# Kernel tuning notes

Measured on AMD Instinct MI355X. Metric: run time of the kernel, lower is better.

## Reference

```python
import jax, jax.numpy as jnp
import numpy as np

GAMMA = 0.3      # LinearSpike surrogate slope (Bellec et al. 2018)
TIMESTEPS = 8
DROPOUT = 0.2

@jax.custom_vjp
def spike_fn(mem_thr):
    # forward: Heaviside spike; backward: piecewise-linear surrogate
    return (mem_thr > 0).astype(mem_thr.dtype)

def _spike_fwd(m):
    return (m > 0).astype(m.dtype), m

def _spike_bwd(m, g):
    return (GAMMA * jnp.maximum(1.0 - jnp.abs(m), 0.0) * g,)

spike_fn.defvjp(_spike_fwd, _spike_bwd)

def conv(x, w, stride=1, pad=1):
    return jax.lax.conv_general_dilated(
        x, w, (stride, stride), [(pad, pad), (pad, pad)],
        dimension_numbers=('NCHW', 'OIHW', 'NCHW'))

def avgpool2(x):
    B, C, H, W = x.shape
    return x.reshape(B, C, H // 2, 2, W // 2, 2).mean(axis=(3, 5))

def lif(mem, delta, leak, thr):
    mem = leak * mem + delta                  # leaky integrate
    mem_thr = mem / thr - 1.0                 # normalized membrane
    out = spike_fn(mem_thr)                   # binary spike
    mem = mem - thr * (mem_thr > 0).astype(mem.dtype)  # soft reset
    return mem, out

def setup_inputs() -> dict:
    key = jax.random.key(0)
    ks = jax.random.split(key, 24)
    B = 32
    def w(k, o, i, kh):
        std = float(np.sqrt(2.0 / (kh * kh * o)))  # matches _initialize_weights2
        return jax.random.normal(k, (o, i, kh, kh), jnp.float32) * std
    def mask(k, shape):
        keep = jax.random.bernoulli(k, 1.0 - DROPOUT, shape)
        return keep.astype(jnp.float32) / (1.0 - DROPOUT)
    return {
        'x': jax.random.normal(ks[0], (B, 3, 32, 32), jnp.float32),
        'w_pre0': w(ks[1], 64, 3, 3),
        'w_pre1': w(ks[2], 64, 64, 3),
        'w_pre2': w(ks[3], 64, 64, 3),
        'w1a': w(ks[4], 64, 64, 3),  'w1b': w(ks[5], 64, 64, 3),
        'w2a': w(ks[6], 128, 64, 3), 'w2b': w(ks[7], 128, 128, 3), 'w2i': w(ks[8], 128, 64, 1),
        'w3a': w(ks[9], 256, 128, 3), 'w3b': w(ks[10], 256, 256, 3), 'w3i': w(ks[11], 256, 128, 1),
        'w4a': w(ks[12], 512, 256, 3), 'w4b': w(ks[13], 512, 512, 3), 'w4i': w(ks[14], 512, 256, 1),
        'w_fc': jax.random.normal(ks[15], (10, 512 * 2 * 2), jnp.float32) * 0.01,
        'thr': jnp.ones((11,), jnp.float32),
        'leak': jnp.ones((11,), jnp.float32),
        'mask2': mask(ks[16], (B, 64, 32, 32)),
        'mask5': mask(ks[17], (B, 64, 32, 32)),
        'mask9': mask(ks[18], (B, 64, 16, 16)),
        'mask11': mask(ks[19], (B, 128, 8, 8)),
        'mask13': mask(ks[20], (B, 256, 4, 4)),
        'mask15': mask(ks[21], (B, 512, 2, 2)),
    }

def _forward(x, w_pre0, w_pre1, w_pre2, w1a, w1b, w2a, w2b, w2i,
             w3a, w3b, w3i, w4a, w4b, w4i, w_fc, thr, leak,
             mask2, mask5, mask9, mask11, mask13, mask15):
    B = x.shape[0]
    f32 = jnp.float32
    mems0 = (
        jnp.zeros((B, 64, 32, 32), f32), jnp.zeros((B, 64, 32, 32), f32),
        jnp.zeros((B, 64, 32, 32), f32),
        jnp.zeros((B, 64, 16, 16), f32), jnp.zeros((B, 64, 16, 16), f32),
        jnp.zeros((B, 128, 8, 8), f32), jnp.zeros((B, 128, 8, 8), f32),
        jnp.zeros((B, 256, 4, 4), f32), jnp.zeros((B, 256, 4, 4), f32),
        jnp.zeros((B, 512, 2, 2), f32), jnp.zeros((B, 512, 2, 2), f32),
        jnp.zeros((B, 10), f32),  # output accumulator mem
    )

    def step(carry, _):
        m0, m1, m2, m3, m4, m5, m6, m7, m8, m9, m10, mfc = carry
        # pre_process: (conv->spike->dropout) x2, conv->spike, avgpool2
        m0, o = lif(m0, conv(x, w_pre0), leak[0], thr[0]); o = o * mask2
        m1, o = lif(m1, conv(o, w_pre1), leak[1], thr[1]); o = o * mask5
        m2, o = lif(m2, conv(o, w_pre2), leak[2], thr[2])
        o = avgpool2(o)  # 32x32 -> 16x16
        # layer1 BasicBlock (stride 1, identity shortcut)
        inp = o
        m3, o = lif(m3, conv(inp, w1a), leak[3], thr[3]); o = o * mask9
        m4, o = lif(m4, conv(o, w1b) + inp, leak[4], thr[4])
        # layer2 BasicBlock (stride 2, 1x1 conv shortcut)
        inp = o
        m5, o = lif(m5, conv(inp, w2a, stride=2), leak[5], thr[5]); o = o * mask11
        m6, o = lif(m6, conv(o, w2b) + conv(inp, w2i, stride=2, pad=0), leak[6], thr[6])
        # layer3
        inp = o
        m7, o = lif(m7, conv(inp, w3a, stride=2), leak[7], thr[7]); o = o * mask13
        m8, o = lif(m8, conv(o, w3b) + conv(inp, w3i, stride=2, pad=0), leak[8], thr[8])
        # layer4
        inp = o
        m9, o = lif(m9, conv(inp, w4a, stride=2), leak[9], thr[9]); o = o * mask15
        m10, o = lif(m10, conv(o, w4b) + conv(inp, w4i, stride=2, pad=0), leak[10], thr[10])
        # output layer: pure accumulation of classifier current over timesteps
        mfc = mfc + o.reshape(B, -1) @ w_fc.T
        return (m0, m1, m2, m3, m4, m5, m6, m7, m8, m9, m10, mfc), None

    carry, _ = jax.lax.scan(step, mems0, None, length=TIMESTEPS)
    return carry[-1]  # [B, labels]

def reference(x, w_pre0, w_pre1, w_pre2, w1a, w1b, w2a, w2b, w2i,
              w3a, w3b, w3i, w4a, w4b, w4i, w_fc, thr, leak,
              mask2, mask5, mask9, mask11, mask13, mask15):
    return _forward(x, w_pre0, w_pre1, w_pre2, w1a, w1b, w2a, w2b, w2i,
                    w3a, w3b, w3i, w4a, w4b, w4i, w_fc, thr, leak,
                    mask2, mask5, mask9, mask11, mask13, mask15)
```

## Files before the change

kernel.cpp:

```cpp
#include <hip/hip_runtime.h>

#define BATCH 32

template<int H, int KS>
__global__ __launch_bounds__(256) void conv64_v2(
    const float* __restrict__ in, const float* __restrict__ w,
    float* __restrict__ pbuf)
{
    constexpr int W    = H;
    constexpr int QR   = W / 4;
    constexpr int ROWS = 64 / QR;
    constexpr int RS   = W + 4;
    constexpr int CC   = 8;
    constexpr int PLANE = (ROWS + 2) * RS;
    constexpr int CCT  = 64 / KS;
    constexpr int NCH  = CCT / CC;
    constexpr int NTOT = 32 * 64 * H * W;
    __shared__ float sIn[CC * PLANE];

    const int tid  = threadIdx.x;
    const int b    = blockIdx.x;
    const int rt   = blockIdx.y;
    const int zc   = blockIdx.z;
    const int cg   = zc & 1;
    const int ks   = zc >> 1;
    const int lane = tid & 63;
    const int g    = __builtin_amdgcn_readfirstlane(tid >> 6);
    const int octet = cg * 32 + g * 8;
    const int r    = lane / QR;
    const int wq   = lane % QR;
    const int ho   = rt * ROWS + r;
    const int row0 = rt * ROWS;

    float acc[8][4] = {};
    const size_t in_b = (size_t)b * 64 * H * W;

    for (int ch = 0; ch < NCH; ++ch) {
        const int c0 = ks * CCT + ch * CC;
        if (ch) __syncthreads();
        constexpr int LCNT = CC * (ROWS + 2) * (W + 2);
        for (int i = tid; i < LCNT; i += 256) {
            int c   = i / ((ROWS + 2) * (W + 2));
            int rr  = (i / (W + 2)) % (ROWS + 2);
            int col = i % (W + 2);
            int ih  = row0 + rr - 1;
            int iw  = col - 1;
            float v = 0.f;
            if ((unsigned)ih < (unsigned)H && (unsigned)iw < (unsigned)W)
                v = in[in_b + (size_t)(c0 + c) * H * W + ih * W + iw];
            sIn[c * PLANE + rr * RS + col] = v;
        }
        __syncthreads();

        for (int c = 0; c < CC; ++c) {
            float rv[3][6];
            #pragma unroll
            for (int dr = 0; dr < 3; ++dr) {
                const float* p = &sIn[c * PLANE + (r + dr) * RS + wq * 4];
                float4 a  = *(const float4*)p;
                float2 b2 = *(const float2*)(p + 4);
                rv[dr][0] = a.x;  rv[dr][1] = a.y; rv[dr][2] = a.z; rv[dr][3] = a.w;
                rv[dr][4] = b2.x; rv[dr][5] = b2.y;
            }
            const float* wc = w + ((size_t)octet * 64 + (c0 + c)) * 9;
            #pragma unroll
            for (int j = 0; j < 8; ++j) {
                const float* wk = wc + (size_t)j * 64 * 9;
                float w0 = wk[0], w1 = wk[1], w2 = wk[2];
                float w3 = wk[3], w4 = wk[4], w5 = wk[5];
                float w6 = wk[6], w7 = wk[7], w8 = wk[8];
                #pragma unroll
                for (int k = 0; k < 4; ++k) {
                    acc[j][k] = fmaf(rv[0][k + 0], w0, acc[j][k]);
                    acc[j][k] = fmaf(rv[0][k + 1], w1, acc[j][k]);
                    acc[j][k] = fmaf(rv[0][k + 2], w2, acc[j][k]);
                    acc[j][k] = fmaf(rv[1][k + 0], w3, acc[j][k]);
                    acc[j][k] = fmaf(rv[1][k + 1], w4, acc[j][k]);
                    acc[j][k] = fmaf(rv[1][k + 2], w5, acc[j][k]);
                    acc[j][k] = fmaf(rv[2][k + 0], w6, acc[j][k]);
                    acc[j][k] = fmaf(rv[2][k + 1], w7, acc[j][k]);
                    acc[j][k] = fmaf(rv[2][k + 2], w8, acc[j][k]);
                }
            }
        }
    }

    #pragma unroll
    for (int j = 0; j < 8; ++j) {
        const size_t idx = ((size_t)(b * 64 + octet + j) * H + ho) * W + wq * 4;
        *(float4*)&pbuf[(size_t)ks * NTOT + idx] =
            make_float4(acc[j][0], acc[j][1], acc[j][2], acc[j][3]);
    }
}

template<int CI, int CO, int KS, int RT>
__global__ __launch_bounds__(256) void conv_mid(
    const float* __restrict__ in,
    const float* __restrict__ w,
    float* __restrict__ pbuf)
{
    constexpr int HIN = 16, HOUT = 8;
    constexpr int CC  = CI / KS;
    constexpr int NR  = (RT - 1) * 2 + 3;
    constexpr int BSTR = NR * HIN + 4;
    constexpr int CST  = 32 * BSTR;
    constexpr int NTOT = 32 * CO * HOUT * HOUT;
    __shared__ float sBuf[CC * CST];

    const int tid  = threadIdx.x;
    const int lane = tid & 63;
    const int b    = lane >> 1;
    const int ks   = blockIdx.x;
    const int co_u = __builtin_amdgcn_readfirstlane(blockIdx.y * 4 + (tid >> 6));
    const int r0   = blockIdx.z * RT;
    const int g0   = r0 * 2 - 1;

    for (int i = tid; i < CC * 32 * NR * 4; i += 256) {
        int q  = i % 4;
        int s  = (i / 4) % NR;
        int bb = (i / (4 * NR)) % 32;
        int c  = i / (4 * NR * 32);
        int gr = g0 + s;
        float4 v = make_float4(0.f, 0.f, 0.f, 0.f);
        if ((unsigned)gr < (unsigned)HIN)
            v = *(const float4*)&in[(((size_t)bb * CI + ks * CC + c) * HIN + gr) * HIN + q * 4];
        *(float4*)&sBuf[c * CST + bb * BSTR + s * HIN + q * 4] = v;
    }
    __syncthreads();

    float acc[RT * 8] = {};
    #pragma unroll 2
    for (int c = 0; c < CC; ++c) {
        const float* wk = w + ((size_t)co_u * CI + ks * CC + c) * 9;
        float wr[9];
        #pragma unroll
        for (int q = 0; q < 9; ++q) wr[q] = wk[q];
        float pl[NR * HIN];
        #pragma unroll
        for (int k = 0; k < NR * 4; ++k) {
            float4 v = *(const float4*)&sBuf[c * CST + b * BSTR + k * 4];
            pl[k * 4 + 0] = v.x; pl[k * 4 + 1] = v.y;
            pl[k * 4 + 2] = v.z; pl[k * 4 + 3] = v.w;
        }
        #pragma unroll
        for (int j = 0; j < RT; ++j) {
            #pragma unroll
            for (int ow = 0; ow < 8; ++ow) {
                #pragma unroll
                for (int kh = 0; kh < 3; ++kh) {
                    const int s = 2 * j + kh;
                    #pragma unroll
                    for (int kw = 0; kw < 3; ++kw) {
                        const int iw = 2 * ow - 1 + kw;
                        if (iw < 0 || iw >= HIN) continue;
                        acc[j * 8 + ow] = fmaf(pl[s * HIN + iw], wr[kh * 3 + kw],
                                               acc[j * 8 + ow]);
                    }
                }
            }
        }
    }

    if ((lane & 1) == 0) {
        #pragma unroll
        for (int j = 0; j < RT; ++j) {
            const size_t idx = ((size_t)(b * CO + co_u) * HOUT + r0 + j) * HOUT;
            *(float4*)&pbuf[(size_t)ks * NTOT + idx]     =
                make_float4(acc[j * 8 + 0], acc[j * 8 + 1], acc[j * 8 + 2], acc[j * 8 + 3]);
            *(float4*)&pbuf[(size_t)ks * NTOT + idx + 4] =
                make_float4(acc[j * 8 + 4], acc[j * 8 + 5], acc[j * 8 + 6], acc[j * 8 + 7]);
        }
    }
}

template<int KS>
__global__ __launch_bounds__(256) void conv_l2b(
    const float* __restrict__ in,
    const float* __restrict__ w,
    const float* __restrict__ sc_in,
    const float* __restrict__ sc_w,
    float* __restrict__ pbuf)
{
    constexpr int CI = 128, CO = 128, SC_CI = 64;
    constexpr int CC  = CI / KS;
    constexpr int SCC = SC_CI / KS;
    constexpr int BSTR = 52;
    constexpr int CST  = 32 * BSTR;
    constexpr int BSTRs = 36;
    constexpr int CSTs  = 32 * BSTRs;
    constexpr int NTOT = 32 * CO * 64;
    __shared__ float sBuf[CC * CST];

    const int tid  = threadIdx.x;
    const int lane = tid & 63;
    const int b    = lane >> 1;
    const int co_u = __builtin_amdgcn_readfirstlane(blockIdx.y * 4 + (tid >> 6));
    const int ks   = blockIdx.x;
    const int sp   = blockIdx.z;
    const int r0   = sp * 4;

    for (int i = tid; i < CC * 32 * 12; i += 256) {
        int f4  = i % 2;
        int row = (i / 2) % 6;
        int bb  = (i / 12) % 32;
        int c   = i / 384;
        int gr  = r0 - 1 + row;
        float4 v = make_float4(0.f, 0.f, 0.f, 0.f);
        if ((unsigned)gr < 8u)
            v = *(const float4*)&in[(((size_t)bb * CI + ks * CC + c) * 8 + gr) * 8 + f4 * 4];
        *(float4*)&sBuf[c * CST + bb * BSTR + row * 8 + f4 * 4] = v;
    }
    __syncthreads();

    float acc[32] = {};
    #pragma unroll 2
    for (int c = 0; c < CC; ++c) {
        const float* wk = w + ((size_t)co_u * CI + ks * CC + c) * 9;
        float wr[9];
        #pragma unroll
        for (int q = 0; q < 9; ++q) wr[q] = wk[q];
        float pl[48];
        #pragma unroll
        for (int k = 0; k < 12; ++k) {
            float4 v = *(const float4*)&sBuf[c * CST + b * BSTR + k * 4];
            pl[k * 4 + 0] = v.x; pl[k * 4 + 1] = v.y;
            pl[k * 4 + 2] = v.z; pl[k * 4 + 3] = v.w;
        }
        #pragma unroll
        for (int oh = 0; oh < 4; ++oh) {
            #pragma unroll
            for (int ow = 0; ow < 8; ++ow) {
                #pragma unroll
                for (int kh = 0; kh < 3; ++kh) {
                    #pragma unroll
                    for (int kw = 0; kw < 3; ++kw) {
                        const int iw = ow - 1 + kw;
                        if (iw < 0 || iw >= 8) continue;
                        acc[oh * 8 + ow] = fmaf(pl[(oh + kh) * 8 + iw],
                                                wr[kh * 3 + kw], acc[oh * 8 + ow]);
                    }
                }
            }
        }
    }
    __syncthreads();

    for (int i = tid; i < SCC * 32 * 16; i += 256) {
        int q   = i % 4;
        int row = (i / 4) % 4;
        int bb  = (i / 16) % 32;
        int c   = i / 512;
        float4 v = *(const float4*)&sc_in[
            (((size_t)bb * SC_CI + ks * SCC + c) * 16 + 2 * (r0 + row)) * 16 + q * 4];
        sBuf[c * CSTs + bb * BSTRs + row * 8 + q * 2 + 0] = v.x;
        sBuf[c * CSTs + bb * BSTRs + row * 8 + q * 2 + 1] = v.z;
    }
    __syncthreads();

    #pragma unroll
    for (int c = 0; c < SCC; ++c) {
        float sw = sc_w[(size_t)co_u * SC_CI + ks * SCC + c];
        #pragma unroll
        for (int p4 = 0; p4 < 8; ++p4) {
            float4 v = *(const float4*)&sBuf[c * CSTs + b * BSTRs + p4 * 4];
            acc[p4 * 4 + 0] = fmaf(v.x, sw, acc[p4 * 4 + 0]);
            acc[p4 * 4 + 1] = fmaf(v.y, sw, acc[p4 * 4 + 1]);
            acc[p4 * 4 + 2] = fmaf(v.z, sw, acc[p4 * 4 + 2]);
            acc[p4 * 4 + 3] = fmaf(v.w, sw, acc[p4 * 4 + 3]);
        }
    }

    if ((lane & 1) == 0) {
        #pragma unroll
        for (int oh = 0; oh < 4; ++oh) {
            const size_t idx = ((size_t)(b * CO + co_u) * 8 + r0 + oh) * 8;
            *(float4*)&pbuf[(size_t)ks * NTOT + idx]     =
                make_float4(acc[oh * 8 + 0], acc[oh * 8 + 1], acc[oh * 8 + 2], acc[oh * 8 + 3]);
            *(float4*)&pbuf[(size_t)ks * NTOT + idx + 4] =
                make_float4(acc[oh * 8 + 4], acc[oh * 8 + 5], acc[oh * 8 + 6], acc[oh * 8 + 7]);
        }
    }
}

template<int CI, int HIN, int STRIDE, int CO, int SC_CI, int SC_HIN,
         int KS, int COB>
__global__ __launch_bounds__(COB * 64) void conv_ks(
    const float* __restrict__ in, const float* __restrict__ w,
    const float* __restrict__ sc_in, const float* __restrict__ sc_w,
    float* __restrict__ pbuf)
{
    constexpr int NT   = COB * 64;
    constexpr int HOUT = (STRIDE == 2) ? HIN / 2 : HIN;
    constexpr int P    = HOUT * HOUT;
    constexpr int NPIX = HIN * HIN;
    constexpr int CC   = CI / KS;
    constexpr int SCC  = (SC_CI > 0) ? SC_CI / KS : 0;
    constexpr int BSTR = NPIX + (((NPIX / 4) % 2 == 0) ? 4 : 0);
    constexpr int CST  = 32 * BSTR;
    constexpr int BSTRs = P + (((P / 4) % 2 == 0) ? 4 : 0);
    constexpr int CSTs  = 32 * BSTRs;
    static_assert(CI % KS == 0, "ks split");
    static_assert(NPIX % 4 == 0 && P % 4 == 0, "vector widths");

    __shared__ float sIn[CC * CST];
    __shared__ float sSc[(SCC > 0) ? SCC * CSTs : 1];

    const int tid  = threadIdx.x;
    const int lane = tid & 63;
    const int b    = lane >> 1;
    const int ks   = blockIdx.x;
    const int co_u = __builtin_amdgcn_readfirstlane(blockIdx.y * COB + (tid >> 6));
    const int cb   = ks * CC;

    constexpr int NF4 = CC * 32 * (NPIX / 4);
    for (int i = tid; i < NF4; i += NT) {
        int k4 = i % (NPIX / 4);
        int c  = (i / (NPIX / 4)) % CC;
        int bb = i / ((NPIX / 4) * CC);
        float4 v = *(const float4*)&in[((size_t)bb * CI + cb + c) * NPIX + k4 * 4];
        *(float4*)&sIn[c * CST + bb * BSTR + k4 * 4] = v;
    }
    if constexpr (SCC > 0) {
        constexpr int NH  = HOUT / 2;
        constexpr int NSC = SCC * 32 * HOUT * NH;
        for (int i = tid; i < NSC; i += NT) {
            int hc = i % NH;
            int r  = (i / NH) % HOUT;
            int c  = (i / (NH * HOUT)) % SCC;
            int bb = i / (NH * HOUT * SCC);
            float4 v = *(const float4*)&sc_in[
                ((size_t)(bb * SC_CI + ks * SCC + c) * SC_HIN + 2 * r) * SC_HIN
                + hc * 4];
            sSc[c * CSTs + bb * BSTRs + r * HOUT + hc * 2 + 0] = v.x;
            sSc[c * CSTs + bb * BSTRs + r * HOUT + hc * 2 + 1] = v.z;
        }
    }
    __syncthreads();

    float acc[P] = {};

    const float* wbase = w + ((size_t)co_u * CI + cb) * 9;
    #pragma unroll 4
    for (int j = 0; j < CC; ++j) {
        float wr[9];
        #pragma unroll
        for (int q = 0; q < 9; ++q) wr[q] = wbase[j * 9 + q];
        float plane[NPIX];
        #pragma unroll
        for (int r4 = 0; r4 < NPIX / 4; ++r4) {
            float4 v = *(const float4*)&sIn[j * CST + b * BSTR + r4 * 4];
            plane[r4 * 4 + 0] = v.x; plane[r4 * 4 + 1] = v.y;
            plane[r4 * 4 + 2] = v.z; plane[r4 * 4 + 3] = v.w;
        }
        #pragma unroll
        for (int ho = 0; ho < HOUT; ++ho) {
            #pragma unroll
            for (int wo = 0; wo < HOUT; ++wo) {
                #pragma unroll
                for (int kh = 0; kh < 3; ++kh) {
                    const int ih = ho * STRIDE - 1 + kh;
                    if (ih < 0 || ih >= HIN) continue;
                    #pragma unroll
                    for (int kw = 0; kw < 3; ++kw) {
                        const int iw = wo * STRIDE - 1 + kw;
                        if (iw < 0 || iw >= HIN) continue;
                        acc[ho * HOUT + wo] =
                            fmaf(plane[ih * HIN + iw], wr[kh * 3 + kw],
                                 acc[ho * HOUT + wo]);
                    }
                }
            }
        }
    }

    if constexpr (SCC > 0) {
        const float* swb = sc_w + (size_t)co_u * SC_CI + ks * SCC;
        #pragma unroll 4
        for (int j = 0; j < SCC; ++j) {
            float sw = swb[j];
            #pragma unroll
            for (int p4 = 0; p4 < P / 4; ++p4) {
                float4 v = *(const float4*)&sSc[j * CSTs + b * BSTRs + p4 * 4];
                acc[p4 * 4 + 0] = fmaf(v.x, sw, acc[p4 * 4 + 0]);
                acc[p4 * 4 + 1] = fmaf(v.y, sw, acc[p4 * 4 + 1]);
                acc[p4 * 4 + 2] = fmaf(v.z, sw, acc[p4 * 4 + 2]);
                acc[p4 * 4 + 3] = fmaf(v.w, sw, acc[p4 * 4 + 3]);
            }
        }
    }

    if ((lane & 1) == 0) {
        float* pp = pbuf + (((size_t)ks * 32 + b) * CO + co_u) * P;
        #pragma unroll
        for (int p4 = 0; p4 < P / 4; ++p4)
            *(float4*)&pp[p4 * 4] = make_float4(acc[p4 * 4], acc[p4 * 4 + 1],
                                                acc[p4 * 4 + 2], acc[p4 * 4 + 3]);
    }
}

template<int CO, int P, int KS>
__global__ __launch_bounds__(256) void reduce_lif(
    const float* __restrict__ pbuf,
    const float* __restrict__ res,
    float* __restrict__ mem,
    const float* __restrict__ thr_a, const float* __restrict__ leak_a, int layer,
    const float* __restrict__ mask, float* __restrict__ out,
    float* __restrict__ accum)
{
    constexpr int TOT4 = 32 * CO * P / 4;
    const int i4 = blockIdx.x * 256 + threadIdx.x;
    if (i4 >= TOT4) return;
    const float4* pb4 = (const float4*)pbuf;
    float4 s = pb4[i4];
    #pragma unroll 4
    for (int ks = 1; ks < KS; ++ks) {
        float4 v = pb4[(size_t)ks * TOT4 + i4];
        s.x += v.x; s.y += v.y; s.z += v.z; s.w += v.w;
    }
    const size_t idx = (size_t)i4 * 4;
    if (res) {
        float4 r4 = *(const float4*)&res[idx];
        s.x += r4.x; s.y += r4.y; s.z += r4.z; s.w += r4.w;
    }
    const float thr  = thr_a[layer];
    const float leak = leak_a[layer];
    float4 m4 = *(const float4*)&mem[idx];
    float4 k4 = mask ? *(const float4*)&mask[idx] : make_float4(1.f, 1.f, 1.f, 1.f);
    float4 mo, oo;
    float m0 = fmaf(leak, m4.x, s.x); float s0 = (m0 / thr - 1.0f > 0.f) ? 1.f : 0.f;
    mo.x = m0 - thr * s0; oo.x = s0 * k4.x;
    float m1 = fmaf(leak, m4.y, s.y); float s1 = (m1 / thr - 1.0f > 0.f) ? 1.f : 0.f;
    mo.y = m1 - thr * s1; oo.y = s1 * k4.y;
    float m2 = fmaf(leak, m4.z, s.z); float s2 = (m2 / thr - 1.0f > 0.f) ? 1.f : 0.f;
    mo.z = m2 - thr * s2; oo.z = s2 * k4.z;
    float m3 = fmaf(leak, m4.w, s.w); float s3 = (m3 / thr - 1.0f > 0.f) ? 1.f : 0.f;
    mo.w = m3 - thr * s3; oo.w = s3 * k4.w;
    *(float4*)&mem[idx] = mo;
    *(float4*)&out[idx] = oo;
    if (accum) {
        float4 a4 = *(const float4*)&accum[idx];
        a4.x += oo.x; a4.y += oo.y; a4.z += oo.z; a4.w += oo.w;
        *(float4*)&accum[idx] = a4;
    }
}

__global__ __launch_bounds__(256) void conv_raw_kernel(
    const float* __restrict__ in, const float* __restrict__ w,
    float* __restrict__ out,
    int Ci, int Co, int Hin, int Win, int total)
{
    int idx = blockIdx.x * blockDim.x + threadIdx.x;
    if (idx >= total) return;
    int wo = idx % Win;
    int t  = idx / Win;
    int ho = t % Hin; t /= Hin;
    int co = t % Co;
    int b  = t / Co;
    int ih0 = ho - 1, iw0 = wo - 1;
    const float* wp = w + (size_t)co * Ci * 9;
    const float* ip = in + (size_t)b * Ci * Hin * Win;
    bool hv0 = (unsigned)(ih0)     < (unsigned)Hin;
    bool hv1 = (unsigned)(ih0 + 1) < (unsigned)Hin;
    bool hv2 = (unsigned)(ih0 + 2) < (unsigned)Hin;
    bool wv0 = (unsigned)(iw0)     < (unsigned)Win;
    bool wv1 = (unsigned)(iw0 + 1) < (unsigned)Win;
    bool wv2 = (unsigned)(iw0 + 2) < (unsigned)Win;
    float acc = 0.f;
    int plane = Hin * Win;
    for (int ci = 0; ci < Ci; ++ci) {
        const float* irow = ip + ci * plane;
        const float* wk   = wp + ci * 9;
        if (hv0) {
            const float* r = irow + ih0 * Win;
            if (wv0) acc = fmaf(r[iw0],     wk[0], acc);
            if (wv1) acc = fmaf(r[iw0 + 1], wk[1], acc);
            if (wv2) acc = fmaf(r[iw0 + 2], wk[2], acc);
        }
        if (hv1) {
            const float* r = irow + (ih0 + 1) * Win;
            if (wv0) acc = fmaf(r[iw0],     wk[3], acc);
            if (wv1) acc = fmaf(r[iw0 + 1], wk[4], acc);
            if (wv2) acc = fmaf(r[iw0 + 2], wk[5], acc);
        }
        if (hv2) {
            const float* r = irow + (ih0 + 2) * Win;
            if (wv0) acc = fmaf(r[iw0],     wk[6], acc);
            if (wv1) acc = fmaf(r[iw0 + 1], wk[7], acc);
            if (wv2) acc = fmaf(r[iw0 + 2], wk[8], acc);
        }
    }
    out[idx] = acc;
}

__global__ __launch_bounds__(256) void lif0_kernel(
    const float4* __restrict__ delta, float4* __restrict__ mem,
    const float* __restrict__ thr_a, const float* __restrict__ leak_a,
    const float4* __restrict__ mask, float4* __restrict__ out, int total4)
{
    int i = blockIdx.x * blockDim.x + threadIdx.x;
    if (i >= total4) return;
    float thr = thr_a[0], leak = leak_a[0];
    float4 d = delta[i], m4 = mem[i], k4 = mask[i], mo, oo;
    float m0 = fmaf(leak, m4.x, d.x); float s0 = (m0 / thr - 1.0f > 0.f) ? 1.f : 0.f;
    mo.x = m0 - thr * s0; oo.x = s0 * k4.x;
    float m1 = fmaf(leak, m4.y, d.y); float s1 = (m1 / thr - 1.0f > 0.f) ? 1.f : 0.f;
    mo.y = m1 - thr * s1; oo.y = s1 * k4.y;
    float m2 = fmaf(leak, m4.z, d.z); float s2 = (m2 / thr - 1.0f > 0.f) ? 1.f : 0.f;
    mo.z = m2 - thr * s2; oo.z = s2 * k4.z;
    float m3 = fmaf(leak, m4.w, d.w); float s3 = (m3 / thr - 1.0f > 0.f) ? 1.f : 0.f;
    mo.w = m3 - thr * s3; oo.w = s3 * k4.w;
    mem[i] = mo; out[i] = oo;
}

__global__ __launch_bounds__(256) void avgpool_kernel(
    const float* __restrict__ in, float* __restrict__ out,
    int C, int Hout, int Wout, int total)
{
    int idx = blockIdx.x * blockDim.x + threadIdx.x;
    if (idx >= total) return;
    int wo = idx % Wout;
    int t  = idx / Wout;
    int ho = t % Hout; t /= Hout;
    int c  = t % C;
    int b  = t / C;
    int Hin = Hout * 2, Win = Wout * 2;
    const float* p = in + (((size_t)b * C + c) * Hin + 2 * ho) * Win + 2 * wo;
    out[idx] = (p[0] + p[1] + p[Win] + p[Win + 1]) * 0.25f;
}

__global__ __launch_bounds__(64) void fc_kernel(
    const float* __restrict__ s, const float* __restrict__ wfc,
    float* __restrict__ out)
{
    int bk = blockIdx.x;
    int b = bk / 10, k = bk % 10;
    const float* sp = s   + (size_t)b * 2048;
    const float* wp = wfc + (size_t)k * 2048;
    float acc = 0.f;
    for (int j = threadIdx.x; j < 2048; j += 64)
        acc = fmaf(sp[j], wp[j], acc);
    #pragma unroll
    for (int off = 32; off; off >>= 1)
        acc += __shfl_down(acc, off, 64);
    if (threadIdx.x == 0) out[b * 10 + k] = acc;
}

extern "C" void kernel_launch(void* const* d_in, const int* in_sizes, int n_in,
                              void* d_out, int out_size, void* d_ws, size_t ws_size,
                              hipStream_t stream) {
    const float* x      = (const float*)d_in[0];
    const float* w_pre0 = (const float*)d_in[1];
    const float* w_pre1 = (const float*)d_in[2];
    const float* w_pre2 = (const float*)d_in[3];
    const float* w1a    = (const float*)d_in[4];
    const float* w1b    = (const float*)d_in[5];
    const float* w2a    = (const float*)d_in[6];
    const float* w2b    = (const float*)d_in[7];
    const float* w2i    = (const float*)d_in[8];
    const float* w3a    = (const float*)d_in[9];
    const float* w3b    = (const float*)d_in[10];
    const float* w3i    = (const float*)d_in[11];
    const float* w4a    = (const float*)d_in[12];
    const float* w4b    = (const float*)d_in[13];
    const float* w4i    = (const float*)d_in[14];
    const float* w_fc   = (const float*)d_in[15];
    const float* thr    = (const float*)d_in[16];
    const float* leak   = (const float*)d_in[17];
    const float* mask2  = (const float*)d_in[18];
    const float* mask5  = (const float*)d_in[19];
    const float* mask9  = (const float*)d_in[20];
    const float* mask11 = (const float*)d_in[21];
    const float* mask13 = (const float*)d_in[22];
    const float* mask15 = (const float*)d_in[23];

    float* ws = (float*)d_ws;
    size_t off = 0;
    auto alloc = [&](size_t n) { float* p = ws + off; off += n; return p; };
    float* m0  = alloc(2097152);
    float* m1  = alloc(2097152);
    float* m2  = alloc(2097152);
    float* m3  = alloc(524288);
    float* m4  = alloc(524288);
    float* m5  = alloc(262144);
    float* m6  = alloc(262144);
    float* m7  = alloc(131072);
    float* m8  = alloc(131072);
    float* m9  = alloc(65536);
    float* m10 = alloc(65536);
    float* ssum = alloc(65536);
    size_t zero_floats = off;
    float* delta0  = alloc(2097152);
    float* s32_a   = alloc(2097152);
    float* s32_b   = alloc(2097152);
    float* s16_inp = alloc(524288);
    float* s16_a   = alloc(524288);
    float* s16_b   = alloc(524288);
    float* s8_a    = alloc(262144);
    float* s8_b    = alloc(262144);
    float* s4_a    = alloc(131072);
    float* s4_b    = alloc(131072);
    float* s2_a    = alloc(65536);
    float* s2_b    = alloc(65536);
    float* pbuf    = alloc(8388608);
    (void)ws_size; (void)in_sizes; (void)n_in; (void)out_size;

    hipMemsetAsync(d_ws, 0, zero_floats * sizeof(float), stream);

    auto grid = [](int total) { return dim3((total + 255) / 256); };

    {
        int total = BATCH * 64 * 32 * 32;
        conv_raw_kernel<<<grid(total), 256, 0, stream>>>(
            x, w_pre0, delta0, 3, 64, 32, 32, total);
    }

    for (int t = 0; t < 8; ++t) {
        int n32 = BATCH * 64 * 32 * 32;
        lif0_kernel<<<grid(n32 / 4), 256, 0, stream>>>(
            (const float4*)delta0, (float4*)m0, thr, leak,
            (const float4*)mask2, (float4*)s32_a, n32 / 4);
        conv64_v2<32, 4><<<dim3(BATCH, 4, 8), 256, 0, stream>>>(s32_a, w_pre1, pbuf);
        reduce_lif<64, 1024, 4><<<dim3(2048), 256, 0, stream>>>(
            pbuf, nullptr, m1, thr, leak, 1, mask5, s32_b, nullptr);
        conv64_v2<32, 4><<<dim3(BATCH, 4, 8), 256, 0, stream>>>(s32_b, w_pre2, pbuf);
        reduce_lif<64, 1024, 4><<<dim3(2048), 256, 0, stream>>>(
            pbuf, nullptr, m2, thr, leak, 2, nullptr, s32_a, nullptr);
        int n16 = BATCH * 64 * 16 * 16;
        avgpool_kernel<<<grid(n16), 256, 0, stream>>>(s32_a, s16_inp, 64, 16, 16, n16);
        conv64_v2<16, 8><<<dim3(BATCH, 1, 16), 256, 0, stream>>>(s16_inp, w1a, pbuf);
        reduce_lif<64, 256, 8><<<dim3(512), 256, 0, stream>>>(
            pbuf, nullptr, m3, thr, leak, 3, mask9, s16_a, nullptr);
        conv64_v2<16, 8><<<dim3(BATCH, 1, 16), 256, 0, stream>>>(s16_a, w1b, pbuf);
        reduce_lif<64, 256, 8><<<dim3(512), 256, 0, stream>>>(
            pbuf, s16_inp, m4, thr, leak, 4, nullptr, s16_b, nullptr);

        conv_mid<64, 128, 16, 2><<<dim3(16, 32, 4), 256, 0, stream>>>(
            s16_b, w2a, pbuf);
        reduce_lif<128, 64, 16><<<dim3(256), 256, 0, stream>>>(
            pbuf, nullptr, m5, thr, leak, 5, mask11, s8_a, nullptr);
        conv_l2b<16><<<dim3(16, 32, 2), 256, 0, stream>>>(
            s8_a, w2b, s16_b, w2i, pbuf);
        reduce_lif<128, 64, 16><<<dim3(256), 256, 0, stream>>>(
            pbuf, nullptr, m6, thr, leak, 6, nullptr, s8_b, nullptr);
        conv_ks<128, 8, 2, 256, 0, 0, 32, 4><<<dim3(32, 64), 256, 0, stream>>>(
            s8_b, w3a, nullptr, nullptr, pbuf);
        reduce_lif<256, 16, 32><<<dim3(128), 256, 0, stream>>>(
            pbuf, nullptr, m7, thr, leak, 7, mask13, s4_a, nullptr);
        conv_ks<256, 4, 1, 256, 128, 8, 16, 4><<<dim3(16, 64), 256, 0, stream>>>(
            s4_a, w3b, s8_b, w3i, pbuf);
        reduce_lif<256, 16, 16><<<dim3(128), 256, 0, stream>>>(
            pbuf, nullptr, m8, thr, leak, 8, nullptr, s4_b, nullptr);
        conv_ks<256, 4, 2, 512, 0, 0, 16, 4><<<dim3(16, 128), 256, 0, stream>>>(
            s4_b, w4a, nullptr, nullptr, pbuf);
        reduce_lif<512, 4, 16><<<dim3(64), 256, 0, stream>>>(
            pbuf, nullptr, m9, thr, leak, 9, mask15, s2_a, nullptr);
        conv_ks<512, 2, 1, 512, 256, 4, 16, 4><<<dim3(16, 128), 256, 0, stream>>>(
            s2_a, w4b, s4_b, w4i, pbuf);
        reduce_lif<512, 4, 16><<<dim3(64), 256, 0, stream>>>(
            pbuf, nullptr, m10, thr, leak, 10, nullptr, s2_b, ssum);
    }

    fc_kernel<<<dim3(320), dim3(64), 0, stream>>>(ssum, w_fc, (float*)d_out);
}
```

Measured before the change: 2.850 ms.

## Double split-K for 64-channel convs and fuse avgpool into LIF reduction

Doubles the channel split (KS 4→8 at 32x32, 8→16 at 16x16) for the 64-channel conv layers, launching twice as many blocks. The pbuf partial-sum buffer grows to match. A new reduce_lif_pool kernel fuses the layer-2 split-K reduction and LIF update with the 2x2 average pool, which removes one launch and a full write and read of the 32x32 spike tensor. More split-K partials add reduction traffic and fewer channels per block lower reuse, in exchange for more parallelism.

```diff
diff --git a/kernel.cpp b/kernel.cpp
--- a/kernel.cpp
+++ b/kernel.cpp
@@ -1,6 +1,8 @@
 #include <hip/hip_runtime.h>
 
 #define BATCH 32
+
+__device__ __forceinline__ float4 ld4(const float* p) { return *(const float4*)p; }
 
 template<int H, int KS>
 __global__ __launch_bounds__(256) void conv64_v2(
@@ -11,10 +13,10 @@
     constexpr int QR   = W / 4;
     constexpr int ROWS = 64 / QR;
     constexpr int RS   = W + 4;
-    constexpr int CC   = 8;
+    constexpr int CCT  = 64 / KS;
+    constexpr int CC   = (CCT < 8) ? CCT : 8;
+    constexpr int NCH  = CCT / CC;
     constexpr int PLANE = (ROWS + 2) * RS;
-    constexpr int CCT  = 64 / KS;
-    constexpr int NCH  = CCT / CC;
     constexpr int NTOT = 32 * 64 * H * W;
     __shared__ float sIn[CC * PLANE];
 
@@ -57,7 +59,7 @@
             #pragma unroll
             for (int dr = 0; dr < 3; ++dr) {
                 const float* p = &sIn[c * PLANE + (r + dr) * RS + wq * 4];
-                float4 a  = *(const float4*)p;
+                float4 a  = ld4(p);
                 float2 b2 = *(const float2*)(p + 4);
                 rv[dr][0] = a.x;  rv[dr][1] = a.y; rv[dr][2] = a.z; rv[dr][3] = a.w;
                 rv[dr][4] = b2.x; rv[dr][5] = b2.y;
@@ -95,8 +97,7 @@
 
 template<int CI, int CO, int KS, int RT>
 __global__ __launch_bounds__(256) void conv_mid(
-    const float* __restrict__ in,
-    const float* __restrict__ w,
+    const float* __restrict__ in, const float* __restrict__ w,
     float* __restrict__ pbuf)
 {
     constexpr int HIN = 16, HOUT = 8;
@@ -123,7 +124,7 @@
         int gr = g0 + s;
         float4 v = make_float4(0.f, 0.f, 0.f, 0.f);
         if ((unsigned)gr < (unsigned)HIN)
-            v = *(const float4*)&in[(((size_t)bb * CI + ks * CC + c) * HIN + gr) * HIN + q * 4];
+            v = ld4(&in[(((size_t)bb * CI + ks * CC + c) * HIN + gr) * HIN + q * 4]);
         *(float4*)&sBuf[c * CST + bb * BSTR + s * HIN + q * 4] = v;
     }
     __syncthreads();
@@ -138,7 +139,7 @@
         float pl[NR * HIN];
         #pragma unroll
         for (int k = 0; k < NR * 4; ++k) {
-            float4 v = *(const float4*)&sBuf[c * CST + b * BSTR + k * 4];
+            float4 v = ld4(&sBuf[c * CST + b * BSTR + k * 4]);
             pl[k * 4 + 0] = v.x; pl[k * 4 + 1] = v.y;
             pl[k * 4 + 2] = v.z; pl[k * 4 + 3] = v.w;
         }
@@ -165,7 +166,7 @@
         #pragma unroll
         for (int j = 0; j < RT; ++j) {
             const size_t idx = ((size_t)(b * CO + co_u) * HOUT + r0 + j) * HOUT;
-            *(float4*)&pbuf[(size_t)ks * NTOT + idx]     =
+            *(float4*)&pbuf[(size_t)ks * NTOT + idx] =
                 make_float4(acc[j * 8 + 0], acc[j * 8 + 1], acc[j * 8 + 2], acc[j * 8 + 3]);
             *(float4*)&pbuf[(size_t)ks * NTOT + idx + 4] =
                 make_float4(acc[j * 8 + 4], acc[j * 8 + 5], acc[j * 8 + 6], acc[j * 8 + 7]);
@@ -184,10 +185,8 @@
     constexpr int CI = 128, CO = 128, SC_CI = 64;
     constexpr int CC  = CI / KS;
     constexpr int SCC = SC_CI / KS;
-    constexpr int BSTR = 52;
-    constexpr int CST  = 32 * BSTR;
-    constexpr int BSTRs = 36;
-    constexpr int CSTs  = 32 * BSTRs;
+    constexpr int BSTR = 52, CST = 32 * BSTR;
+    constexpr int BSTRs = 36, CSTs = 32 * BSTRs;
     constexpr int NTOT = 32 * CO * 64;
     __shared__ float sBuf[CC * CST];
 
@@ -196,8 +195,7 @@
     const int b    = lane >> 1;
     const int co_u = __builtin_amdgcn_readfirstlane(blockIdx.y * 4 + (tid >> 6));
     const int ks   = blockIdx.x;
-    const int sp   = blockIdx.z;
-    const int r0   = sp * 4;
+    const int r0   = blockIdx.z * 4;
 
     for (int i = tid; i < CC * 32 * 12; i += 256) {
         int f4  = i % 2;
@@ -207,7 +205,7 @@
         int gr  = r0 - 1 + row;
         float4 v = make_float4(0.f, 0.f, 0.f, 0.f);
         if ((unsigned)gr < 8u)
-            v = *(const float4*)&in[(((size_t)bb * CI + ks * CC + c) * 8 + gr) * 8 + f4 * 4];
+            v = ld4(&in[(((size_t)bb * CI + ks * CC + c) * 8 + gr) * 8 + f4 * 4]);
         *(float4*)&sBuf[c * CST + bb * BSTR + row * 8 + f4 * 4] = v;
     }
     __syncthreads();
@@ -222,7 +220,7 @@
         float pl[48];
         #pragma unroll
         for (int k = 0; k < 12; ++k) {
-            float4 v = *(const float4*)&sBuf[c * CST + b * BSTR + k * 4];
+            float4 v = ld4(&sBuf[c * CST + b * BSTR + k * 4]);
             pl[k * 4 + 0] = v.x; pl[k * 4 + 1] = v.y;
             pl[k * 4 + 2] = v.z; pl[k * 4 + 3] = v.w;
         }
@@ -250,8 +248,8 @@
         int row = (i / 4) % 4;
         int bb  = (i / 16) % 32;
         int c   = i / 512;
-        float4 v = *(const float4*)&sc_in[
-            (((size_t)bb * SC_CI + ks * SCC + c) * 16 + 2 * (r0 + row)) * 16 + q * 4];
+        float4 v = ld4(&sc_in[
+            (((size_t)bb * SC_CI + ks * SCC + c) * 16 + 2 * (r0 + row)) * 16 + q * 4]);
         sBuf[c * CSTs + bb * BSTRs + row * 8 + q * 2 + 0] = v.x;
         sBuf[c * CSTs + bb * BSTRs + row * 8 + q * 2 + 1] = v.z;
     }
@@ -262,7 +260,7 @@
         float sw = sc_w[(size_t)co_u * SC_CI + ks * SCC + c];
         #pragma unroll
         for (int p4 = 0; p4 < 8; ++p4) {
-            float4 v = *(const float4*)&sBuf[c * CSTs + b * BSTRs + p4 * 4];
+            float4 v = ld4(&sBuf[c * CSTs + b * BSTRs + p4 * 4]);
             acc[p4 * 4 + 0] = fmaf(v.x, sw, acc[p4 * 4 + 0]);
             acc[p4 * 4 + 1] = fmaf(v.y, sw, acc[p4 * 4 + 1]);
             acc[p4 * 4 + 2] = fmaf(v.z, sw, acc[p4 * 4 + 2]);
@@ -317,7 +315,7 @@
         int k4 = i % (NPIX / 4);
         int c  = (i / (NPIX / 4)) % CC;
         int bb = i / ((NPIX / 4) * CC);
-        float4 v = *(const float4*)&in[((size_t)bb * CI + cb + c) * NPIX + k4 * 4];
+        float4 v = ld4(&in[((size_t)bb * CI + cb + c) * NPIX + k4 * 4]);
         *(float4*)&sIn[c * CST + bb * BSTR + k4 * 4] = v;
     }
     if constexpr (SCC > 0) {
@@ -328,9 +326,9 @@
             int r  = (i / NH) % HOUT;
             int c  = (i / (NH * HOUT)) % SCC;
             int bb = i / (NH * HOUT * SCC);
-            float4 v = *(const float4*)&sc_in[
+            float4 v = ld4(&sc_in[
                 ((size_t)(bb * SC_CI + ks * SCC + c) * SC_HIN + 2 * r) * SC_HIN
-                + hc * 4];
+                + hc * 4]);
             sSc[c * CSTs + bb * BSTRs + r * HOUT + hc * 2 + 0] = v.x;
             sSc[c * CSTs + bb * BSTRs + r * HOUT + hc * 2 + 1] = v.z;
         }
@@ -348,7 +346,7 @@
         float plane[NPIX];
         #pragma unroll
         for (int r4 = 0; r4 < NPIX / 4; ++r4) {
-            float4 v = *(const float4*)&sIn[j * CST + b * BSTR + r4 * 4];
+            float4 v = ld4(&sIn[j * CST + b * BSTR + r4 * 4]);
             plane[r4 * 4 + 0] = v.x; plane[r4 * 4 + 1] = v.y;
             plane[r4 * 4 + 2] = v.z; plane[r4 * 4 + 3] = v.w;
         }
@@ -380,7 +378,7 @@
             float sw = swb[j];
             #pragma unroll
             for (int p4 = 0; p4 < P / 4; ++p4) {
-                float4 v = *(const float4*)&sSc[j * CSTs + b * BSTRs + p4 * 4];
+                float4 v = ld4(&sSc[j * CSTs + b * BSTRs + p4 * 4]);
                 acc[p4 * 4 + 0] = fmaf(v.x, sw, acc[p4 * 4 + 0]);
                 acc[p4 * 4 + 1] = fmaf(v.y, sw, acc[p4 * 4 + 1]);
                 acc[p4 * 4 + 2] = fmaf(v.z, sw, acc[p4 * 4 + 2]);
@@ -419,13 +417,13 @@
     }
     const size_t idx = (size_t)i4 * 4;
     if (res) {
-        float4 r4 = *(const float4*)&res[idx];
+        float4 r4 = ld4(&res[idx]);
         s.x += r4.x; s.y += r4.y; s.z += r4.z; s.w += r4.w;
     }
     const float thr  = thr_a[layer];
     const float leak = leak_a[layer];
-    float4 m4 = *(const float4*)&mem[idx];
-    float4 k4 = mask ? *(const float4*)&mask[idx] : make_float4(1.f, 1.f, 1.f, 1.f);
+    float4 m4 = ld4(&mem[idx]);
+    float4 k4 = mask ? ld4(&mask[idx]) : make_float4(1.f, 1.f, 1.f, 1.f);
     float4 mo, oo;
     float m0 = fmaf(leak, m4.x, s.x); float s0 = (m0 / thr - 1.0f > 0.f) ? 1.f : 0.f;
     mo.x = m0 - thr * s0; oo.x = s0 * k4.x;
@@ -438,10 +436,64 @@
     *(float4*)&mem[idx] = mo;
     *(float4*)&out[idx] = oo;
     if (accum) {
-        float4 a4 = *(const float4*)&accum[idx];
+        float4 a4 = ld4(&accum[idx]);
         a4.x += oo.x; a4.y += oo.y; a4.z += oo.z; a4.w += oo.w;
         *(float4*)&accum[idx] = a4;
     }
+}
+
+template<int KS>
+__global__ __launch_bounds__(256) void reduce_lif_pool(
+    const float* __restrict__ pbuf, float* __restrict__ mem,
+    const float* __restrict__ thr_a, const float* __restrict__ leak_a, int layer,
+    float* __restrict__ pool_out)
+{
+    constexpr int TOT = 32 * 64 * 32 * 32;
+    const int i = blockIdx.x * 256 + threadIdx.x;
+    const int q  = i % 8;
+    const int rp = (i / 8) % 16;
+    const int c  = (i / 128) % 64;
+    const int b  = i / 8192;
+    const size_t idx0 = (((size_t)(b * 64 + c) * 32) + 2 * rp) * 32 + 4 * q;
+    const size_t idx1 = idx0 + 32;
+
+    float4 s0 = ld4(&pbuf[idx0]);
+    float4 s1 = ld4(&pbuf[idx1]);
+    #pragma unroll 4
+    for (int ks = 1; ks < KS; ++ks) {
+        float4 v0 = ld4(&pbuf[(size_t)ks * TOT + idx0]);
+        float4 v1 = ld4(&pbuf[(size_t)ks * TOT + idx1]);
+        s0.x += v0.x; s0.y += v0.y; s0.z += v0.z; s0.w += v0.w;
+        s1.x += v1.x; s1.y += v1.y; s1.z += v1.z; s1.w += v1.w;
+    }
+    const float thr  = thr_a[layer];
+    const float leak = leak_a[layer];
+    float4 m0 = ld4(&mem[idx0]), m1 = ld4(&mem[idx1]);
+    float4 n0, n1, o0, o1;
+    {
+        float m = fmaf(leak, m0.x, s0.x); float sp = (m / thr - 1.0f > 0.f) ? 1.f : 0.f;
+        n0.x = m - thr * sp; o0.x = sp;
+        m = fmaf(leak, m0.y, s0.y); sp = (m / thr - 1.0f > 0.f) ? 1.f : 0.f;
+        n0.y = m - thr * sp; o0.y = sp;
+        m = fmaf(leak, m0.z, s0.z); sp = (m / thr - 1.0f > 0.f) ? 1.f : 0.f;
+        n0.z = m - thr * sp; o0.z = sp;
+        m = fmaf(leak, m0.w, s0.w); sp = (m / thr - 1.0f > 0.f) ? 1.f : 0.f;
+        n0.w = m - thr * sp; o0.w = sp;
+        m = fmaf(leak, m1.x, s1.x); sp = (m / thr - 1.0f > 0.f) ? 1.f : 0.f;
+        n1.x = m - thr * sp; o1.x = sp;
+        m = fmaf(leak, m1.y, s1.y); sp = (m / thr - 1.0f > 0.f) ? 1.f : 0.f;
+        n1.y = m - thr * sp; o1.y = sp;
+        m = fmaf(leak, m1.z, s1.z); sp = (m / thr - 1.0f > 0.f) ? 1.f : 0.f;
+        n1.z = m - thr * sp; o1.z = sp;
+        m = fmaf(leak, m1.w, s1.w); sp = (m / thr - 1.0f > 0.f) ? 1.f : 0.f;
+        n1.w = m - thr * sp; o1.w = sp;
+    }
+    *(float4*)&mem[idx0] = n0;
+    *(float4*)&mem[idx1] = n1;
+    float2 pv;
+    pv.x = (o0.x + o0.y + o1.x + o1.y) * 0.25f;
+    pv.y = (o0.z + o0.w + o1.z + o1.w) * 0.25f;
+    *(float2*)&pool_out[(((size_t)(b * 64 + c) * 16) + rp) * 16 + 2 * q] = pv;
 }
 
 __global__ __launch_bounds__(256) void conv_raw_kernel(
@@ -510,22 +562,6 @@
     float m3 = fmaf(leak, m4.w, d.w); float s3 = (m3 / thr - 1.0f > 0.f) ? 1.f : 0.f;
     mo.w = m3 - thr * s3; oo.w = s3 * k4.w;
     mem[i] = mo; out[i] = oo;
-}
-
-__global__ __launch_bounds__(256) void avgpool_kernel(
-    const float* __restrict__ in, float* __restrict__ out,
-    int C, int Hout, int Wout, int total)
-{
-    int idx = blockIdx.x * blockDim.x + threadIdx.x;
-    if (idx >= total) return;
-    int wo = idx % Wout;
-    int t  = idx / Wout;
-    int ho = t % Hout; t /= Hout;
-    int c  = t % C;
-    int b  = t / C;
-    int Hin = Hout * 2, Win = Wout * 2;
-    const float* p = in + (((size_t)b * C + c) * Hin + 2 * ho) * Win + 2 * wo;
-    out[idx] = (p[0] + p[1] + p[Win] + p[Win + 1]) * 0.25f;
 }
 
 __global__ __launch_bounds__(64) void fc_kernel(
@@ -601,7 +637,7 @@
     float* s4_b    = alloc(131072);
     float* s2_a    = alloc(65536);
     float* s2_b    = alloc(65536);
-    float* pbuf    = alloc(8388608);
+    float* pbuf    = alloc(16777216);
     (void)ws_size; (void)in_sizes; (void)n_in; (void)out_size;
 
     hipMemsetAsync(d_ws, 0, zero_floats * sizeof(float), stream);
@@ -619,19 +655,17 @@
         lif0_kernel<<<grid(n32 / 4), 256, 0, stream>>>(
             (const float4*)delta0, (float4*)m0, thr, leak,
             (const float4*)mask2, (float4*)s32_a, n32 / 4);
-        conv64_v2<32, 4><<<dim3(BATCH, 4, 8), 256, 0, stream>>>(s32_a, w_pre1, pbuf);
-        reduce_lif<64, 1024, 4><<<dim3(2048), 256, 0, stream>>>(
+        conv64_v2<32, 8><<<dim3(BATCH, 4, 16), 256, 0, stream>>>(s32_a, w_pre1, pbuf);
+        reduce_lif<64, 1024, 8><<<dim3(2048), 256, 0, stream>>>(
             pbuf, nullptr, m1, thr, leak, 1, mask5, s32_b, nullptr);
-        conv64_v2<32, 4><<<dim3(BATCH, 4, 8), 256, 0, stream>>>(s32_b, w_pre2, pbuf);
-        reduce_lif<64, 1024, 4><<<dim3(2048), 256, 0, stream>>>(
-            pbuf, nullptr, m2, thr, leak, 2, nullptr, s32_a, nullptr);
-        int n16 = BATCH * 64 * 16 * 16;
-        avgpool_kernel<<<grid(n16), 256, 0, stream>>>(s32_a, s16_inp, 64, 16, 16, n16);
-        conv64_v2<16, 8><<<dim3(BATCH, 1, 16), 256, 0, stream>>>(s16_inp, w1a, pbuf);
-        reduce_lif<64, 256, 8><<<dim3(512), 256, 0, stream>>>(
+        conv64_v2<32, 8><<<dim3(BATCH, 4, 16), 256, 0, stream>>>(s32_b, w_pre2, pbuf);
+        reduce_lif_pool<8><<<dim3(1024), 256, 0, stream>>>(
+            pbuf, m2, thr, leak, 2, s16_inp);
+        conv64_v2<16, 16><<<dim3(BATCH, 1, 32), 256, 0, stream>>>(s16_inp, w1a, pbuf);
+        reduce_lif<64, 256, 16><<<dim3(512), 256, 0, stream>>>(
             pbuf, nullptr, m3, thr, leak, 3, mask9, s16_a, nullptr);
-        conv64_v2<16, 8><<<dim3(BATCH, 1, 16), 256, 0, stream>>>(s16_a, w1b, pbuf);
-        reduce_lif<64, 256, 8><<<dim3(512), 256, 0, stream>>>(
+        conv64_v2<16, 16><<<dim3(BATCH, 1, 32), 256, 0, stream>>>(s16_a, w1b, pbuf);
+        reduce_lif<64, 256, 16><<<dim3(512), 256, 0, stream>>>(
             pbuf, s16_inp, m4, thr, leak, 4, nullptr, s16_b, nullptr);
 
         conv_mid<64, 128, 16, 2><<<dim3(16, 32, 4), 256, 0, stream>>>(
```

After: 2.885 ms. Within noise of the previous version (+1.2%).
